# Optimization experiments

Hardware: AMD Instinct MI355X
Metric: run time of the kernel (lower is better)

Reference implementation:

```python
import jax, jax.numpy as jnp
import numpy as np
import math

N_HEADS = 16  # matches init_kwargs n_heads


def setup_inputs() -> dict:
    key = jax.random.key(0)
    k1, k2, k3 = jax.random.split(key, 3)
    B, S, D = 8, 1024, 1024
    x = jax.random.normal(k1, (B, S, D), dtype=jnp.float32)
    Wc = jax.random.normal(k2, (D, 3 * D), dtype=jnp.float32) * 0.02
    bc = jnp.zeros((3 * D,), dtype=jnp.float32)
    Wo = jax.random.normal(k3, (D, D), dtype=jnp.float32) * 0.02
    bo = jnp.zeros((D,), dtype=jnp.float32)
    return {"x": x, "Wc": Wc, "bc": bc, "Wo": Wo, "bo": bo}


def reference(x, Wc, bc, Wo, bo):
    B, S, D = x.shape
    H = N_HEADS
    hd = D // H
    qkv = x @ Wc + bc                         # [B,S,3D]
    q, k, v = jnp.split(qkv, 3, axis=2)
    q = q.reshape(B, S, H, hd)
    k = k.reshape(B, S, H, hd)
    v = v.reshape(B, S, H, hd)
    # NOTE: source scales by sqrt(d_size), not sqrt(head_dim)
    scores = jnp.einsum("bqhd,bkhd->bhqk", q, k) / math.sqrt(D)
    # source mask: triu(ones) kept, zeros (k < q) filled with float32 min
    # i.e. attend only to positions k >= q (anti-causal, faithful to source)
    keep = jnp.triu(jnp.ones((S, S), dtype=bool))  # [S,S]
    neg = jnp.finfo(jnp.float32).min
    scores = jnp.where(keep[None, None, :, :], scores, neg)
    attn = jax.nn.softmax(scores, axis=-1)    # [B,H,S,S]; dropout p=0 -> identity
    out = jnp.einsum("bhqk,bkhd->bqhd", attn, v)
    concat = out.reshape(B, S, D)
    return concat @ Wo + bo                   # final dropout p=0 -> identity
```

## Files before the change

### kernel.cpp

```cpp
#include <hip/hip_runtime.h>
#include <stdint.h>

typedef __attribute__((ext_vector_type(8))) short  bf16x8;
typedef __attribute__((ext_vector_type(4))) short  short4v;
typedef __attribute__((ext_vector_type(4))) float  f32x4;
typedef __attribute__((ext_vector_type(4))) float  float4v;

#define VMW(N) asm volatile("s_waitcnt vmcnt(" #N ")" ::: "memory")
#define BAR()  asm volatile("s_barrier" ::: "memory")

__device__ __forceinline__ short f2bf(float f) {
  union { float f; uint32_t u; } c; c.f = f;
  uint32_t u = c.u;
  uint32_t r = (u + 0x7FFFu + ((u >> 16) & 1u)) >> 16;
  return (short)(uint16_t)r;
}

__device__ __forceinline__ short f2bf_hw(float f) {
  return __builtin_bit_cast(short, (__bf16)f);
}

__device__ __forceinline__ void gload_lds16(const void* g, void* l) {
  __builtin_amdgcn_global_load_lds(
      (const __attribute__((address_space(1))) void*)g,
      (__attribute__((address_space(3))) void*)l, 16, 0, 0);
}

__global__ __launch_bounds__(256) void k_f32_to_bf16(
    const float* __restrict__ in, short* __restrict__ out, int n4) {
  const int stride = gridDim.x * 256;
  for (int i = blockIdx.x * 256 + threadIdx.x; i < n4; i += stride) {
    float4v v = *(const float4v*)(in + (size_t)i * 4);
    short4v o;
    o.x = f2bf(v.x); o.y = f2bf(v.y); o.z = f2bf(v.z); o.w = f2bf(v.w);
    *(short4v*)(out + (size_t)i * 4) = o;
  }
}

__global__ __launch_bounds__(256) void k_transpose_bf16(
    const float* __restrict__ in, short* __restrict__ out, int R, int C) {
  __shared__ short tile[64][65];
  int bc = blockIdx.x * 64, br = blockIdx.y * 64;
  int tc = threadIdx.x & 63, tr = threadIdx.x >> 6;
#pragma unroll
  for (int i = 0; i < 64; i += 4)
    tile[tc][tr + i] = f2bf(in[(size_t)(br + tr + i) * C + bc + tc]);
  __syncthreads();
#pragma unroll
  for (int i = 0; i < 64; i += 4)
    out[(size_t)(bc + tr + i) * R + br + tc] = tile[tr + i][tc];
}

template <bool F32OUT>
__global__ __launch_bounds__(256) void k_gemm2(
    const short* __restrict__ A, const short* __restrict__ BT,
    const float* __restrict__ bias, void* __restrict__ Cout,
    int M, int N, int K, int nbn) {
  __shared__ short SM[2][2][2][128][32];
  const int tid = threadIdx.x;
  const int w = tid >> 6, l = tid & 63;
  const int fr = l & 15, fg = l >> 4;
  const int wm = w >> 1, wn = w & 1;

  const int q8 = gridDim.x >> 3;
  const int wg = (blockIdx.x & 7) * q8 + (blockIdx.x >> 3);
  const int bm = wg / nbn, bn = wg % nbn;
  const size_t brow = (size_t)bm << 7;
  const int bcol = bn << 7;

  const int NT = K >> 6;

  const int srow = l >> 2;
  const int soct = (l & 3) ^ ((l >> 3) & 3);
  const short* aG = A + (brow + srow) * (size_t)K + soct * 8;
  const short* bG = BT + ((size_t)(bcol + srow)) * K + soct * 8;
  const int slot8 = ((fg ^ ((fr >> 1) & 3)) << 3);

  f32x4 acc[4][4] = {};

#pragma unroll
  for (int s = 0; s < 6; ++s) {
    const int t = s >> 2, tau = s & 3, buf = t & 1, mat = tau & 1, kh = tau >> 1;
    const int kbase = t * 64 + kh * 32;
    const short* g0 = (mat ? bG : aG) + kbase;
#pragma unroll
    for (int j = 0; j < 2; ++j) {
      const int r0 = (w * 2 + j) * 16;
      gload_lds16(g0 + (size_t)r0 * K, (char*)&SM[buf][mat][kh][r0][0]);
    }
  }
  VMW(8);
  BAR();

  int sidx = 6;
  for (int t = 0; t < NT; ++t) {
    const int buf = t & 1;
#pragma unroll
    for (int p = 0; p < 2; ++p) {
      const int kh = p;
#pragma unroll
      for (int s = 0; s < 2; ++s) {
        if (sidx < NT * 4) {
          const int ts = sidx >> 2, tau = sidx & 3;
          const int sb = ts & 1, mat = tau & 1, skh = tau >> 1;
          const int kbase = ts * 64 + skh * 32;
          const short* g0 = (mat ? bG : aG) + kbase;
#pragma unroll
          for (int j = 0; j < 2; ++j) {
            const int r0 = (w * 2 + j) * 16;
            gload_lds16(g0 + (size_t)r0 * K, (char*)&SM[sb][mat][skh][r0][0]);
          }
          ++sidx;
        }
      }
      bf16x8 af[4], bf[4];
#pragma unroll
      for (int m = 0; m < 4; ++m)
        af[m] = *(const bf16x8*)&SM[buf][0][kh][wm * 64 + m * 16 + fr][slot8];
#pragma unroll
      for (int n = 0; n < 4; ++n)
        bf[n] = *(const bf16x8*)&SM[buf][1][kh][wn * 64 + n * 16 + fr][slot8];
      BAR();
      __builtin_amdgcn_s_setprio(1);
#pragma unroll
      for (int m = 0; m < 4; ++m)
#pragma unroll
        for (int n = 0; n < 4; ++n)
          acc[m][n] = __builtin_amdgcn_mfma_f32_16x16x32_bf16(
              af[m], bf[n], acc[m][n], 0, 0, 0);
      __builtin_amdgcn_s_setprio(0);
      if (!(t == NT - 1 && p == 1)) {
        if (t == NT - 1 && p == 0) { VMW(0); }
        else if (t == NT - 2 && p == 1) { VMW(4); }
        else { VMW(8); }
        BAR();
      }
    }
  }

#pragma unroll
  for (int n = 0; n < 4; ++n) {
    const int col = bcol + wn * 64 + n * 16 + fr;
    const float bv = bias[col];
#pragma unroll
    for (int i = 0; i < 4; ++i) {
      const size_t row = brow + (size_t)(wm * 64 + i * 16 + fg * 4);
#pragma unroll
      for (int r = 0; r < 4; ++r) {
        const float v = acc[i][n][r] + bv;
        if (F32OUT)
          ((float*)Cout)[(row + r) * (size_t)N + col] = v;
        else
          ((short*)Cout)[(row + r) * (size_t)N + col] = f2bf(v);
      }
    }
  }
}

__global__ __launch_bounds__(256) void k_attn(
    const short* __restrict__ qkv, short* __restrict__ outc, int Bn, int S) {
  __shared__ short Ks[128][64];
  __shared__ short Vt[64][136];

  const int tid = threadIdx.x;
  const int w = tid >> 6, l = tid & 63;
  const int fr = l & 15, fg = l >> 4;

  const int tq = blockIdx.x >> 7;
  const int bh = blockIdx.x & 127;
  const int h = bh & 15, b = bh >> 4;
  const int q0 = tq << 6;

  const size_t rowbase = (size_t)b * S;
  const int qcol = q0 + w * 16 + fr;

  bf16x8 qf[2];
  {
    const short* qp = qkv + (rowbase + qcol) * 3072 + h * 64 + fg * 8;
    qf[0] = *(const bf16x8*)qp;
    qf[1] = *(const bf16x8*)(qp + 32);
    const float C2 = 0.04508422f;
#pragma unroll
    for (int j = 0; j < 8; ++j) {
      union { float f; uint32_t u; } ca, cb;
      ca.u = ((uint32_t)(uint16_t)qf[0][j]) << 16;
      cb.u = ((uint32_t)(uint16_t)qf[1][j]) << 16;
      qf[0][j] = f2bf_hw(ca.f * C2);
      qf[1][j] = f2bf_hw(cb.f * C2);
    }
  }

  f32x4 o[4] = {};
  float lacc = 0.0f;

  const short* Kbase = qkv + rowbase * 3072 + 1024 + h * 64;
  const short* Vbase = qkv + rowbase * 3072 + 2048 + h * 64;

  const int r8 = l >> 3, slot = l & 7;
  const int vdb = (tid >> 4) << 2;

#define STAGE_K(c)                                                             \
  {                                                                            \
    const int k0s = (c) << 7;                                                  \
    _Pragma("unroll") for (int j = 0; j < 4; ++j) {                            \
      int ch = w * 4 + j;                                                      \
      int row = ch * 8 + r8;                                                   \
      int d = (slot ^ (row & 7)) << 3;                                         \
      gload_lds16(Kbase + (size_t)(k0s + row) * 3072 + d,                      \
                  (char*)&Ks[0][0] + ch * 1024);                               \
    }                                                                          \
  }
#define LOAD_V(c)                                                              \
  {                                                                            \
    const int k0s = (c) << 7;                                                  \
    _Pragma("unroll") for (int kh = 0; kh < 2; ++kh) {                         \
      int kb = ((tid & 15) << 2) + (kh << 6);                                  \
      const short* vp = Vbase + (size_t)(k0s + kb) * 3072 + vdb;               \
      vr[kh][0] = *(const short4v*)(vp);                                       \
      vr[kh][1] = *(const short4v*)(vp + 3072);                                \
      vr[kh][2] = *(const short4v*)(vp + 2 * 3072);                            \
      vr[kh][3] = *(const short4v*)(vp + 3 * 3072);                            \
    }                                                                          \
  }

  const int c0 = tq >> 1;
  short4v vr[2][4];
  STAGE_K(c0);
  LOAD_V(c0);

  for (int c = c0; c < 8; ++c) {
    const int k0 = c << 7;
    VMW(0);
    __syncthreads();

#pragma unroll
    for (int kh = 0; kh < 2; ++kh) {
      int kb = ((tid & 15) << 2) + (kh << 6);
      short4v t0 = {vr[kh][0].x, vr[kh][1].x, vr[kh][2].x, vr[kh][3].x};
      short4v t1 = {vr[kh][0].y, vr[kh][1].y, vr[kh][2].y, vr[kh][3].y};
      short4v t2 = {vr[kh][0].z, vr[kh][1].z, vr[kh][2].z, vr[kh][3].z};
      short4v t3 = {vr[kh][0].w, vr[kh][1].w, vr[kh][2].w, vr[kh][3].w};
      *(short4v*)&Vt[vdb + 0][kb] = t0;
      *(short4v*)&Vt[vdb + 1][kb] = t1;
      *(short4v*)&Vt[vdb + 2][kb] = t2;
      *(short4v*)&Vt[vdb + 3][kb] = t3;
    }

    f32x4 st[8];
#pragma unroll
    for (int kb = 0; kb < 8; ++kb) {
      f32x4 z = {0.f, 0.f, 0.f, 0.f};
      int row = kb * 16 + fr;
      int sw = row & 7;
      bf16x8 kf0 = *(const bf16x8*)&Ks[row][(fg ^ sw) << 3];
      bf16x8 kf1 = *(const bf16x8*)&Ks[row][((4 + fg) ^ sw) << 3];
      z = __builtin_amdgcn_mfma_f32_16x16x32_bf16(kf0, qf[0], z, 0, 0, 0);
      z = __builtin_amdgcn_mfma_f32_16x16x32_bf16(kf1, qf[1], z, 0, 0, 0);
      st[kb] = z;
    }

    if (c + 1 < 8) LOAD_V(c + 1);

    const bool masked = (c == c0);
#pragma unroll
    for (int kb = 0; kb < 8; ++kb)
#pragma unroll
      for (int r = 0; r < 4; ++r) {
        float e = exp2f(st[kb][r]);
        if (masked) {
          int kg = k0 + kb * 16 + fg * 4 + r;
          e = (kg < qcol) ? 0.0f : e;
        }
        st[kb][r] = e;
        lacc += e;
      }

    __syncthreads();

    if (c + 1 < 8) STAGE_K(c + 1);

#pragma unroll
    for (int kb2 = 0; kb2 < 4; ++kb2) {
      bf16x8 pa = {f2bf_hw(st[2 * kb2][0]),     f2bf_hw(st[2 * kb2][1]),
                   f2bf_hw(st[2 * kb2][2]),     f2bf_hw(st[2 * kb2][3]),
                   f2bf_hw(st[2 * kb2 + 1][0]), f2bf_hw(st[2 * kb2 + 1][1]),
                   f2bf_hw(st[2 * kb2 + 1][2]), f2bf_hw(st[2 * kb2 + 1][3])};
#pragma unroll
      for (int f = 0; f < 4; ++f) {
        short4v v0 = *(const short4v*)&Vt[f * 16 + fr][kb2 * 32 + fg * 4];
        short4v v1 = *(const short4v*)&Vt[f * 16 + fr][kb2 * 32 + 16 + fg * 4];
        bf16x8 vb = {v0.x, v0.y, v0.z, v0.w, v1.x, v1.y, v1.z, v1.w};
        o[f] = __builtin_amdgcn_mfma_f32_16x16x32_bf16(pa, vb, o[f], 0, 0, 0);
      }
    }
  }
#undef STAGE_K
#undef LOAD_V

  lacc += __shfl_xor(lacc, 16, 64);
  lacc += __shfl_xor(lacc, 32, 64);
#pragma unroll
  for (int r = 0; r < 4; ++r) {
    float denom = __shfl(lacc, fg * 4 + r, 64);
    float inv = 1.0f / denom;
    size_t orow = rowbase + (size_t)(q0 + w * 16 + fg * 4 + r);
    short* op = outc + orow * 1024 + h * 64 + fr;
#pragma unroll
    for (int f = 0; f < 4; ++f) op[f * 16] = f2bf(o[f][r] * inv);
  }
}

extern "C" void kernel_launch(void* const* d_in, const int* in_sizes, int n_in,
                              void* d_out, int out_size, void* d_ws,
                              size_t ws_size, hipStream_t stream) {
  const float* x = (const float*)d_in[0];
  const float* Wc = (const float*)d_in[1];
  const float* bc = (const float*)d_in[2];
  const float* Wo = (const float*)d_in[3];
  const float* bo = (const float*)d_in[4];
  float* out = (float*)d_out;

  const int Bn = 8, S = 1024, D = 1024;
  const int M = Bn * S;

  char* ws = (char*)d_ws;
  short* xb  = (short*)(ws);
  short* wct = (short*)(ws + (size_t)16 * 1024 * 1024);
  short* wot = (short*)(ws + (size_t)22 * 1024 * 1024);
  short* qkv = (short*)(ws + (size_t)24 * 1024 * 1024);
  short* cat = (short*)(ws + (size_t)72 * 1024 * 1024);

  k_f32_to_bf16<<<2048, 256, 0, stream>>>(x, xb, M * D / 4);
  {
    dim3 g(3 * D / 64, D / 64);
    k_transpose_bf16<<<g, 256, 0, stream>>>(Wc, wct, D, 3 * D);
  }
  {
    dim3 g(D / 64, D / 64);
    k_transpose_bf16<<<g, 256, 0, stream>>>(Wo, wot, D, D);
  }
  k_gemm2<false><<<(M / 128) * (3 * D / 128), 256, 0, stream>>>(
      xb, wct, bc, qkv, M, 3 * D, D, 3 * D / 128);
  k_attn<<<16 * 128, 256, 0, stream>>>(qkv, cat, Bn, S);
  k_gemm2<true><<<(M / 128) * (D / 128), 256, 0, stream>>>(
      cat, wot, bo, out, M, D, D, D / 128);
}
```

Baseline: 162.7 us.

## Pair complementary query tiles per attention block and fuse prep kernels

Each attention block now handles two query tiles, j and 15-j, so every block does an equal amount of anti-causal work and shares each staged K/V chunk between both tiles. This cuts the grid from 2048 to 1024 blocks and removes the load imbalance between short and long rows. The three preprocessing kernels (x conversion and two weight transposes) are merged into one launch to save launch overhead. In exchange the attention kernel holds twice the Q fragments and accumulators, which raises register pressure and may lower occupancy.

```diff
diff --git a/kernel.cpp b/kernel.cpp
--- a/kernel.cpp
+++ b/kernel.cpp
@@ -26,21 +26,10 @@
       (__attribute__((address_space(3))) void*)l, 16, 0, 0);
 }
 
-__global__ __launch_bounds__(256) void k_f32_to_bf16(
-    const float* __restrict__ in, short* __restrict__ out, int n4) {
-  const int stride = gridDim.x * 256;
-  for (int i = blockIdx.x * 256 + threadIdx.x; i < n4; i += stride) {
-    float4v v = *(const float4v*)(in + (size_t)i * 4);
-    short4v o;
-    o.x = f2bf(v.x); o.y = f2bf(v.y); o.z = f2bf(v.z); o.w = f2bf(v.w);
-    *(short4v*)(out + (size_t)i * 4) = o;
-  }
-}
-
-__global__ __launch_bounds__(256) void k_transpose_bf16(
-    const float* __restrict__ in, short* __restrict__ out, int R, int C) {
-  __shared__ short tile[64][65];
-  int bc = blockIdx.x * 64, br = blockIdx.y * 64;
+__device__ __forceinline__ void transpose_body(
+    const float* __restrict__ in, short* __restrict__ out, int R, int C,
+    int bx, int by, short (*tile)[65]) {
+  int bc = bx * 64, br = by * 64;
   int tc = threadIdx.x & 63, tr = threadIdx.x >> 6;
 #pragma unroll
   for (int i = 0; i < 64; i += 4)
@@ -49,6 +38,29 @@
 #pragma unroll
   for (int i = 0; i < 64; i += 4)
     out[(size_t)(bc + tr + i) * R + br + tc] = tile[tr + i][tc];
+}
+
+__global__ __launch_bounds__(256) void k_prep(
+    const float* __restrict__ x, short* __restrict__ xb, int n4,
+    const float* __restrict__ Wc, short* __restrict__ wct,
+    const float* __restrict__ Wo, short* __restrict__ wot) {
+  __shared__ short tile[64][65];
+  const int id = blockIdx.x;
+  if (id < 1024) {
+    const int stride = 1024 * 256;
+    for (int i = id * 256 + threadIdx.x; i < n4; i += stride) {
+      float4v v = *(const float4v*)(x + (size_t)i * 4);
+      short4v o;
+      o.x = f2bf(v.x); o.y = f2bf(v.y); o.z = f2bf(v.z); o.w = f2bf(v.w);
+      *(short4v*)(xb + (size_t)i * 4) = o;
+    }
+  } else if (id < 1024 + 768) {
+    int t = id - 1024;
+    transpose_body(Wc, wct, 1024, 3072, t % 48, t / 48, tile);
+  } else {
+    int t = id - 1792;
+    transpose_body(Wo, wot, 1024, 1024, t & 15, t >> 4, tile);
+  }
 }
 
 template <bool F32OUT>
@@ -166,32 +178,39 @@
   const int w = tid >> 6, l = tid & 63;
   const int fr = l & 15, fg = l >> 4;
 
-  const int tq = blockIdx.x >> 7;
+  const int j = blockIdx.x >> 7;
   const int bh = blockIdx.x & 127;
   const int h = bh & 15, b = bh >> 4;
-  const int q0 = tq << 6;
+  const int tqa = j, tqb = 15 - j;
+  const int q0a = tqa << 6, q0b = tqb << 6;
 
   const size_t rowbase = (size_t)b * S;
-  const int qcol = q0 + w * 16 + fr;
-
-  bf16x8 qf[2];
+  const int qcola = q0a + w * 16 + fr;
+  const int qcolb = q0b + w * 16 + fr;
+
+  bf16x8 qfa[2], qfb[2];
   {
-    const short* qp = qkv + (rowbase + qcol) * 3072 + h * 64 + fg * 8;
-    qf[0] = *(const bf16x8*)qp;
-    qf[1] = *(const bf16x8*)(qp + 32);
     const float C2 = 0.04508422f;
-#pragma unroll
-    for (int j = 0; j < 8; ++j) {
-      union { float f; uint32_t u; } ca, cb;
-      ca.u = ((uint32_t)(uint16_t)qf[0][j]) << 16;
-      cb.u = ((uint32_t)(uint16_t)qf[1][j]) << 16;
-      qf[0][j] = f2bf_hw(ca.f * C2);
-      qf[1][j] = f2bf_hw(cb.f * C2);
-    }
-  }
-
-  f32x4 o[4] = {};
-  float lacc = 0.0f;
+    const short* qp = qkv + (rowbase + qcola) * 3072 + h * 64 + fg * 8;
+    const short* qq = qkv + (rowbase + qcolb) * 3072 + h * 64 + fg * 8;
+    qfa[0] = *(const bf16x8*)qp;  qfa[1] = *(const bf16x8*)(qp + 32);
+    qfb[0] = *(const bf16x8*)qq;  qfb[1] = *(const bf16x8*)(qq + 32);
+#pragma unroll
+    for (int i = 0; i < 8; ++i) {
+      union { float f; uint32_t u; } c0, c1, c2, c3;
+      c0.u = ((uint32_t)(uint16_t)qfa[0][i]) << 16;
+      c1.u = ((uint32_t)(uint16_t)qfa[1][i]) << 16;
+      c2.u = ((uint32_t)(uint16_t)qfb[0][i]) << 16;
+      c3.u = ((uint32_t)(uint16_t)qfb[1][i]) << 16;
+      qfa[0][i] = f2bf_hw(c0.f * C2);
+      qfa[1][i] = f2bf_hw(c1.f * C2);
+      qfb[0][i] = f2bf_hw(c2.f * C2);
+      qfb[1][i] = f2bf_hw(c3.f * C2);
+    }
+  }
+
+  f32x4 oa[4] = {}, ob[4] = {};
+  float la = 0.0f, lb = 0.0f;
 
   const short* Kbase = qkv + rowbase * 3072 + 1024 + h * 64;
   const short* Vbase = qkv + rowbase * 3072 + 2048 + h * 64;
@@ -202,8 +221,8 @@
 #define STAGE_K(c)                                                             \
   {                                                                            \
     const int k0s = (c) << 7;                                                  \
-    _Pragma("unroll") for (int j = 0; j < 4; ++j) {                            \
-      int ch = w * 4 + j;                                                      \
+    _Pragma("unroll") for (int jj = 0; jj < 4; ++jj) {                         \
+      int ch = w * 4 + jj;                                                     \
       int row = ch * 8 + r8;                                                   \
       int d = (slot ^ (row & 7)) << 3;                                         \
       gload_lds16(Kbase + (size_t)(k0s + row) * 3072 + d,                      \
@@ -222,14 +241,58 @@
       vr[kh][3] = *(const short4v*)(vp + 3 * 3072);                            \
     }                                                                          \
   }
-
-  const int c0 = tq >> 1;
+#define QKSM(qf, qcol, lac, pa, c, cdiag)                                      \
+  {                                                                            \
+    f32x4 st[8];                                                               \
+    _Pragma("unroll") for (int kb = 0; kb < 8; ++kb) {                         \
+      f32x4 z = {0.f, 0.f, 0.f, 0.f};                                          \
+      int row = kb * 16 + fr;                                                  \
+      int sw = row & 7;                                                        \
+      bf16x8 kf0 = *(const bf16x8*)&Ks[row][(fg ^ sw) << 3];                   \
+      bf16x8 kf1 = *(const bf16x8*)&Ks[row][((4 + fg) ^ sw) << 3];             \
+      z = __builtin_amdgcn_mfma_f32_16x16x32_bf16(kf0, qf[0], z, 0, 0, 0);     \
+      z = __builtin_amdgcn_mfma_f32_16x16x32_bf16(kf1, qf[1], z, 0, 0, 0);     \
+      st[kb] = z;                                                              \
+    }                                                                          \
+    const bool masked = ((c) == (cdiag));                                      \
+    const int k0m = (c) << 7;                                                  \
+    _Pragma("unroll") for (int kb = 0; kb < 8; ++kb)                           \
+        _Pragma("unroll") for (int r = 0; r < 4; ++r) {                        \
+      float e = exp2f(st[kb][r]);                                              \
+      if (masked) {                                                            \
+        int kg = k0m + kb * 16 + fg * 4 + r;                                   \
+        e = (kg < (qcol)) ? 0.0f : e;                                          \
+      }                                                                        \
+      st[kb][r] = e;                                                           \
+      lac += e;                                                                \
+    }                                                                          \
+    _Pragma("unroll") for (int kb2 = 0; kb2 < 4; ++kb2) {                      \
+      bf16x8 t = {f2bf_hw(st[2 * kb2][0]),     f2bf_hw(st[2 * kb2][1]),        \
+                  f2bf_hw(st[2 * kb2][2]),     f2bf_hw(st[2 * kb2][3]),        \
+                  f2bf_hw(st[2 * kb2 + 1][0]), f2bf_hw(st[2 * kb2 + 1][1]),    \
+                  f2bf_hw(st[2 * kb2 + 1][2]), f2bf_hw(st[2 * kb2 + 1][3])};   \
+      pa[kb2] = t;                                                             \
+    }                                                                          \
+  }
+#define PV(pa, o)                                                              \
+  {                                                                            \
+    _Pragma("unroll") for (int kb2 = 0; kb2 < 4; ++kb2) {                      \
+      _Pragma("unroll") for (int f = 0; f < 4; ++f) {                          \
+        short4v v0 = *(const short4v*)&Vt[f * 16 + fr][kb2 * 32 + fg * 4];     \
+        short4v v1 = *(const short4v*)&Vt[f * 16 + fr][kb2 * 32 + 16 + fg * 4];\
+        bf16x8 vb = {v0.x, v0.y, v0.z, v0.w, v1.x, v1.y, v1.z, v1.w};          \
+        o[f] = __builtin_amdgcn_mfma_f32_16x16x32_bf16(pa[kb2], vb, o[f], 0, 0, 0); \
+      }                                                                        \
+    }                                                                          \
+  }
+
+  const int c0a = tqa >> 1;
+  const int c0b = tqb >> 1;
   short4v vr[2][4];
-  STAGE_K(c0);
-  LOAD_V(c0);
-
-  for (int c = c0; c < 8; ++c) {
-    const int k0 = c << 7;
+  STAGE_K(c0a);
+  LOAD_V(c0a);
+
+  for (int c = c0a; c < 8; ++c) {
     VMW(0);
     __syncthreads();
 
@@ -246,67 +309,43 @@
       *(short4v*)&Vt[vdb + 3][kb] = t3;
     }
 
-    f32x4 st[8];
-#pragma unroll
-    for (int kb = 0; kb < 8; ++kb) {
-      f32x4 z = {0.f, 0.f, 0.f, 0.f};
-      int row = kb * 16 + fr;
-      int sw = row & 7;
-      bf16x8 kf0 = *(const bf16x8*)&Ks[row][(fg ^ sw) << 3];
-      bf16x8 kf1 = *(const bf16x8*)&Ks[row][((4 + fg) ^ sw) << 3];
-      z = __builtin_amdgcn_mfma_f32_16x16x32_bf16(kf0, qf[0], z, 0, 0, 0);
-      z = __builtin_amdgcn_mfma_f32_16x16x32_bf16(kf1, qf[1], z, 0, 0, 0);
-      st[kb] = z;
-    }
+    const bool doB = (c >= c0b);
+    bf16x8 pa_a[4], pa_b[4];
+    QKSM(qfa, qcola, la, pa_a, c, c0a);
+    if (doB) QKSM(qfb, qcolb, lb, pa_b, c, c0b);
 
     if (c + 1 < 8) LOAD_V(c + 1);
 
-    const bool masked = (c == c0);
-#pragma unroll
-    for (int kb = 0; kb < 8; ++kb)
-#pragma unroll
-      for (int r = 0; r < 4; ++r) {
-        float e = exp2f(st[kb][r]);
-        if (masked) {
-          int kg = k0 + kb * 16 + fg * 4 + r;
-          e = (kg < qcol) ? 0.0f : e;
-        }
-        st[kb][r] = e;
-        lacc += e;
-      }
-
     __syncthreads();
 
     if (c + 1 < 8) STAGE_K(c + 1);
 
-#pragma unroll
-    for (int kb2 = 0; kb2 < 4; ++kb2) {
-      bf16x8 pa = {f2bf_hw(st[2 * kb2][0]),     f2bf_hw(st[2 * kb2][1]),
-                   f2bf_hw(st[2 * kb2][2]),     f2bf_hw(st[2 * kb2][3]),
-                   f2bf_hw(st[2 * kb2 + 1][0]), f2bf_hw(st[2 * kb2 + 1][1]),
-                   f2bf_hw(st[2 * kb2 + 1][2]), f2bf_hw(st[2 * kb2 + 1][3])};
-#pragma unroll
-      for (int f = 0; f < 4; ++f) {
-        short4v v0 = *(const short4v*)&Vt[f * 16 + fr][kb2 * 32 + fg * 4];
-        short4v v1 = *(const short4v*)&Vt[f * 16 + fr][kb2 * 32 + 16 + fg * 4];
-        bf16x8 vb = {v0.x, v0.y, v0.z, v0.w, v1.x, v1.y, v1.z, v1.w};
-        o[f] = __builtin_amdgcn_mfma_f32_16x16x32_bf16(pa, vb, o[f], 0, 0, 0);
-      }
-    }
+    PV(pa_a, oa);
+    if (doB) PV(pa_b, ob);
   }
 #undef STAGE_K
 #undef LOAD_V
-
-  lacc += __shfl_xor(lacc, 16, 64);
-  lacc += __shfl_xor(lacc, 32, 64);
+#undef QKSM
+#undef PV
+
+  la += __shfl_xor(la, 16, 64);
+  la += __shfl_xor(la, 32, 64);
+  lb += __shfl_xor(lb, 16, 64);
+  lb += __shfl_xor(lb, 32, 64);
 #pragma unroll
   for (int r = 0; r < 4; ++r) {
-    float denom = __shfl(lacc, fg * 4 + r, 64);
-    float inv = 1.0f / denom;
-    size_t orow = rowbase + (size_t)(q0 + w * 16 + fg * 4 + r);
-    short* op = outc + orow * 1024 + h * 64 + fr;
-#pragma unroll
-    for (int f = 0; f < 4; ++f) op[f * 16] = f2bf(o[f][r] * inv);
+    float da = __shfl(la, fg * 4 + r, 64);
+    float db = __shfl(lb, fg * 4 + r, 64);
+    float ia = 1.0f / da, ib = 1.0f / db;
+    size_t ra = rowbase + (size_t)(q0a + w * 16 + fg * 4 + r);
+    size_t rb = rowbase + (size_t)(q0b + w * 16 + fg * 4 + r);
+    short* opa = outc + ra * 1024 + h * 64 + fr;
+    short* opb = outc + rb * 1024 + h * 64 + fr;
+#pragma unroll
+    for (int f = 0; f < 4; ++f) {
+      opa[f * 16] = f2bf(oa[f][r] * ia);
+      opb[f * 16] = f2bf(ob[f][r] * ib);
+    }
   }
 }
 
@@ -330,18 +369,10 @@
   short* qkv = (short*)(ws + (size_t)24 * 1024 * 1024);
   short* cat = (short*)(ws + (size_t)72 * 1024 * 1024);
 
-  k_f32_to_bf16<<<2048, 256, 0, stream>>>(x, xb, M * D / 4);
-  {
-    dim3 g(3 * D / 64, D / 64);
-    k_transpose_bf16<<<g, 256, 0, stream>>>(Wc, wct, D, 3 * D);
-  }
-  {
-    dim3 g(D / 64, D / 64);
-    k_transpose_bf16<<<g, 256, 0, stream>>>(Wo, wot, D, D);
-  }
+  k_prep<<<2048, 256, 0, stream>>>(x, xb, M * D / 4, Wc, wct, Wo, wot);
   k_gemm2<false><<<(M / 128) * (3 * D / 128), 256, 0, stream>>>(
       xb, wct, bc, qkv, M, 3 * D, D, 3 * D / 128);
-  k_attn<<<16 * 128, 256, 0, stream>>>(qkv, cat, Bn, S);
+  k_attn<<<8 * 128, 256, 0, stream>>>(qkv, cat, Bn, S);
   k_gemm2<true><<<(M / 128) * (D / 128), 256, 0, stream>>>(
       cat, wot, bo, out, M, D, D, D / 128);
 }
```

New measurement: 192.0 us. +18.0%, slower.
